# Kernel tuning notes

Hardware: AMD Instinct MI355X
Metric: run time of the kernel (lower is better)

The kernel has to match this reference:

```python
import jax, jax.numpy as jnp
import numpy as np

NEG = -1e9  # stands in for float('-inf'); exp(NEG)==0 exactly in fp32, keeps grads NaN-free
EPS = 1e-5  # torch_struct matrix-tree regularizer


def _lstm_bwd_dir(x, lengths, W_ih, W_hh, b_ih, b_hh):
    """Backward direction of a PyTorch bidirectional LSTM over packed sequences.
    x: [N,S,D], lengths: [N]. Returns y: [N,S,H] where y[n,t] is the reverse-direction
    hidden state at position t (zeros for t >= lengths[n], matching pad_packed_sequence)."""
    N, S, D = x.shape
    Hh = W_hh.shape[1]
    k = jnp.arange(S)
    idx = jnp.clip(lengths[:, None] - 1 - k[None, :], 0, S - 1)  # reverse-within-length gather
    valid = k[None, :] < lengths[:, None]                        # [N,S]
    xr = jnp.take_along_axis(x, idx[:, :, None], axis=1) * valid[..., None]

    def step(carry, inp):
        h, c = carry
        xt, vt = inp
        gates = xt @ W_ih.T + h @ W_hh.T + (b_ih + b_hh)
        i, f, g, o = jnp.split(gates, 4, axis=-1)  # PyTorch gate order i,f,g,o
        c_new = jax.nn.sigmoid(f) * c + jax.nn.sigmoid(i) * jnp.tanh(g)
        h_new = jax.nn.sigmoid(o) * jnp.tanh(c_new)
        m = vt[:, None]
        return (jnp.where(m, h_new, h), jnp.where(m, c_new, c)), jnp.where(m, h_new, 0.0)

    init = (jnp.zeros((N, Hh), x.dtype), jnp.zeros((N, Hh), x.dtype))
    _, hr = jax.lax.scan(step, init, (jnp.swapaxes(xr, 0, 1), valid.T))
    hr = jnp.swapaxes(hr, 0, 1)  # [N,S,H], in reversed coordinates
    return jnp.take_along_axis(hr, idx[:, :, None], axis=1) * valid[..., None]


def _contextualize(pv, lengths, pf, pb):
    B, S, _, H = pv.shape
    rows = pv.reshape(B * S, S, H)
    # rows_f: flipped rows, lengths [S, S-1, ..., 1] per batch, rnn_b reverse-dir
    len_rf = jnp.tile(S - jnp.arange(S), B)
    rows_f = jnp.flip(_lstm_bwd_dir(jnp.flip(rows, 1), len_rf, *pb), 1)
    # rows_b: dialogue lengths, rnn_f reverse-dir
    len_rb = jnp.repeat(lengths, S)
    rows_b = _lstm_bwd_dir(rows, len_rb, *pf)
    rows_out = jnp.concatenate([rows_f, rows_b], -1).reshape(B, S, S, 2 * H)
    cols = jnp.swapaxes(pv, 1, 2).reshape(B * S, S, H)
    # cols_b: lengths [1, 2, ..., S] per batch, rnn_b reverse-dir
    len_cb = jnp.tile(jnp.arange(1, S + 1), B)
    cols_b = _lstm_bwd_dir(cols, len_cb, *pb)
    # cols_f: flipped cols, full length S, rnn_f reverse-dir
    len_cf = jnp.full((B * S,), S, dtype=jnp.int32)
    cols_f = jnp.flip(_lstm_bwd_dir(jnp.flip(cols, 1), len_cf, *pf), 1)
    cols_out = jnp.concatenate([cols_f, cols_b], -1).reshape(B, S, S, 2 * H)
    return rows_out + jnp.swapaxes(cols_out, 1, 2)


def _apply_mask(pt, lengths):
    B, T, S, _ = pt.shape
    eye = jnp.eye(S, dtype=bool)
    t_idx = jnp.arange(T)[:, None, None]
    pt = jnp.where((t_idx < T - 1) & eye, NEG, pt)                      # no non-root types on diag
    pt = jnp.where((t_idx == T - 1) & jnp.triu(jnp.ones((S, S), bool), 1), NEG, pt)  # root type only on diag
    col_pad = jnp.arange(S)[None, :] >= lengths[:, None]                 # [B,S]
    pt = jnp.where(col_pad[:, None, None, :], NEG, pt)                   # length mask on columns
    pt = jnp.where(~jnp.triu(jnp.ones((S, S), bool)), NEG, pt)           # only i <= j arcs
    return pt


def _deptree_partition(scores, lengths):
    # matrix-tree theorem partition (torch_struct NonProjectiveDependencyCRF, multiroot)
    B, S, _ = scores.shape
    valid = jnp.arange(S)[None, :] < lengths[:, None]
    scores = jnp.where(valid[:, :, None] & valid[:, None, :], scores, NEG)
    A = jnp.exp(scores) + EPS
    A = jnp.where(jnp.eye(S, dtype=bool), 0.0, A)
    lap = -A + jnp.eye(S, dtype=scores.dtype) * A.sum(axis=1)[:, None, :]  # diag(colsum) - A
    lap = lap.at[:, 0, :].set(jnp.exp(jnp.diagonal(scores, axis1=-2, axis2=-1)))  # root row
    lap = lap + jnp.eye(S, dtype=scores.dtype) * (~valid).astype(scores.dtype)[:, None, :]  # padded dims -> det*1
    return jnp.linalg.slogdet(lap)[1]


def _expand_matrix(pt):
    B, T, S, _ = pt.shape
    m = pt.reshape(B * T, S, S)
    d = jnp.diagonal(m, axis1=-2, axis2=-1)                # [BT,S]
    me = jnp.concatenate([d[:, None, :], m], axis=1)       # [BT,S+1,S]
    pad = jnp.full((B * T, S + 1, 1), NEG, pt.dtype)
    me = jnp.concatenate([pad, me], axis=2)                # [BT,S+1,S+1]
    me = jnp.where(jnp.eye(S + 1, dtype=bool), 0.0, me)
    return me.reshape(B, T, S + 1, S + 1)


def _forward(B, S, lengths, struct_vec, Wih_f, Whh_f, bih_f, bhh_f, Wih_b, Whh_b, bih_b, bhh_b, Wt, bt):
    H = struct_vec.shape[-1]
    ti, tj = np.triu_indices(S)
    pv = jnp.zeros((B, S, S, H), struct_vec.dtype).at[:, ti, tj].set(struct_vec)
    pv = _contextualize(pv, lengths, (Wih_f, Whh_f, bih_f, bhh_f), (Wih_b, Whh_b, bih_b, bhh_b))
    pt = jnp.einsum('bijd,td->btij', pv, Wt) + bt[None, :, None, None]  # Linear + permute(0,3,1,2)
    pt = _apply_mask(pt, lengths)
    labeled = jax.nn.logsumexp(pt, axis=1)                 # [B,S,S]
    logZ = _deptree_partition(labeled, lengths)
    pe = _expand_matrix(pt)
    return pe, logZ


def setup_inputs() -> dict:
    B, S, H, T = 8, 64, 512, 17
    key = jax.random.key(0)
    ks = jax.random.split(key, 12)
    s = 1.0 / np.sqrt(H)
    s2 = 1.0 / np.sqrt(2 * H)
    u = lambda k, shape, sc: jax.random.uniform(k, shape, jnp.float32, -sc, sc)
    return {
        'batch_size': B,
        'seq_len': S,
        'context_sentence_masks': jax.random.randint(ks[0], (B,), S // 2, S + 1),
        'struct_vec': jax.random.normal(ks[1], (B, S * (S + 1) // 2, H), jnp.float32),
        'input_labels': 1,
        'Wih_f': u(ks[2], (4 * H, H), s), 'Whh_f': u(ks[3], (4 * H, H), s),
        'bih_f': u(ks[4], (4 * H,), s), 'bhh_f': u(ks[5], (4 * H,), s),
        'Wih_b': u(ks[6], (4 * H, H), s), 'Whh_b': u(ks[7], (4 * H, H), s),
        'bih_b': u(ks[8], (4 * H,), s), 'bhh_b': u(ks[9], (4 * H,), s),
        'Wt': u(ks[10], (T, 2 * H), s2), 'bt': u(ks[11], (T,), s2),
    }


def reference(batch_size, seq_len, context_sentence_masks, struct_vec, input_labels,
              Wih_f, Whh_f, bih_f, bhh_f, Wih_b, Whh_b, bih_b, bhh_b, Wt, bt):
    return _forward(batch_size, seq_len, context_sentence_masks, struct_vec,
                    Wih_f, Whh_f, bih_f, bhh_f, Wih_b, Whh_b, bih_b, bhh_b, Wt, bt)
```

## Files before the change

kernel.cpp:

```cpp
#include <hip/hip_runtime.h>
#include <hip/hip_bf16.h>
#include <math.h>

#define NEGF (-1000000000.0f)

constexpr int Bc = 8;
constexpr int Sc = 64;
constexpr int Hc = 512;
constexpr int Tc = 17;
constexpr int TRIc = Sc*(Sc+1)/2;
constexpr int PTN  = Bc*Tc*Sc*Sc;

typedef __bf16 bf16x8 __attribute__((ext_vector_type(8)));
typedef float  f32x4  __attribute__((ext_vector_type(4)));

__device__ __forceinline__ int tri_idx(int i, int j){
  return i*Sc - (i*(i-1))/2 + (j - i);
}

__device__ __forceinline__ void posmap(int pass, int r, int k, int L,
                                       int& i, int& j, bool& act){
  if      (pass == 0){ act = (r < L - k);            i = r;     j = L - 1 - k; }
  else if (pass == 1){ act = (r < L - k);            i = r;     j = r + k;     }
  else if (pass == 2){ act = (r >= k) && (r < L);    i = r - k; j = r;         }
  else               { act = (r >= k) && (r < L);    i = k;     j = r;         }
  if (!act){ i = 0; j = 0; }
}

__device__ __forceinline__ float pt_val(const float* __restrict__ pt_acc,
                                        const float* __restrict__ btv,
                                        int b, int t, int i, int j, int L){
  const bool masked = (i > j) || (j >= L) ||
                      (t < Tc-1 && i == j) || (t == Tc-1 && i < j);
  if (masked) return NEGF;
  const size_t idx = (((size_t)b*Tc + t)*Sc + i)*Sc + j;
  return pt_acc[idx] + pt_acc[PTN + idx] + pt_acc[2*PTN + idx]
       + pt_acc[3*PTN + idx] + btv[t];
}

__global__ __launch_bounds__(256) void k_cvt(const float* __restrict__ s,
                                             __hip_bfloat16* __restrict__ d, int n4){
  int i = blockIdx.x*256 + threadIdx.x;
  if (i >= n4) return;
  float4 v = reinterpret_cast<const float4*>(s)[i];
  union { __hip_bfloat16 h[4]; ushort4 u; } p;
  p.h[0] = __float2bfloat16(v.x); p.h[1] = __float2bfloat16(v.y);
  p.h[2] = __float2bfloat16(v.z); p.h[3] = __float2bfloat16(v.w);
  reinterpret_cast<ushort4*>(d)[i] = p.u;
}

__global__ __launch_bounds__(256) void k_pack(
    const float* __restrict__ Whh_f, const float* __restrict__ Wih_f,
    const float* __restrict__ Whh_b, const float* __restrict__ Wih_b,
    __hip_bfloat16* __restrict__ Wp)
{
  int idx = blockIdx.x*256 + threadIdx.x;
  int k4  = idx & 255;
  int row = (idx >> 8) & 63;
  int us  = (idx >> 14) & 31;
  int ws  = idx >> 19;
  int g = row >> 4, uu = row & 15;
  int srow = g*512 + us*16 + uu;
  int k = k4*4;
  const float* src;
  if (ws == 0) src = (k < 512) ? Whh_f : Wih_f;
  else         src = (k < 512) ? Whh_b : Wih_b;
  float4 v = *reinterpret_cast<const float4*>(src + (size_t)srow*512 + (k & 511));
  union { __hip_bfloat16 h[4]; ushort4 u; } p;
  p.h[0] = __float2bfloat16(v.x); p.h[1] = __float2bfloat16(v.y);
  p.h[2] = __float2bfloat16(v.z); p.h[3] = __float2bfloat16(v.w);
  *reinterpret_cast<ushort4*>(Wp + (size_t)idx*4) = p.u;
}

__global__ __launch_bounds__(512) void k_persist(
    const __hip_bfloat16* __restrict__ Wp,
    const float* __restrict__ bih_f, const float* __restrict__ bhh_f,
    const float* __restrict__ bih_b, const float* __restrict__ bhh_b,
    const __hip_bfloat16* __restrict__ svb, const float* __restrict__ Wt,
    const int* __restrict__ lens,
    __hip_bfloat16* __restrict__ H,
    float* __restrict__ pt_acc, int* __restrict__ flags)
{
  const int bid = blockIdx.x;
  const int grp = bid & 7;
  const int us  = bid >> 3;
  const int pp  = grp >> 2;
  const int bq  = grp & 3;
  const int L0 = lens[bq*2], L1 = lens[bq*2+1];
  const int kmax = (L0 > L1) ? L0 : L1;

  const float* b1 = pp ? bih_b : bih_f;
  const float* b2 = pp ? bhh_b : bhh_f;

  const int t = threadIdx.x, lane = t & 63, wv = t >> 6;
  const int c15 = lane & 15, qq = lane >> 4;
  const int ph = wv >> 2;
  const int mq = wv & 3;
  const int pass = pp ? (ph ? 2 : 1) : (ph ? 3 : 0);
  const int b_loc = mq >> 1;
  const int b  = bq*2 + b_loc;
  const int L  = b_loc ? L1 : L0;
  const int rb0 = (mq & 1)*32;

  __shared__ ushort Wlds[65536];

  {
    const __hip_bfloat16* Wpb = Wp + (((size_t)pp*32 + us)*64)*1024;
    const int row = t >> 3, c8 = t & 7;
    const int swz = (row & 7) << 4;
    #pragma unroll
    for (int q=0; q<16; ++q){
      int4 v = *reinterpret_cast<const int4*>(Wpb + (size_t)row*1024 + c8*128 + q*8);
      *reinterpret_cast<int4*>((char*)Wlds + ((row*2048 + c8*256 + q*16) ^ swz)) = v;
    }
  }

  const int u = us*16 + c15;
  const float bsI = b1[u]        + b2[u];
  const float bsF = b1[512 + u]  + b2[512 + u];
  const float bsG = b1[1024 + u] + b2[1024 + u];
  const float bsO = b1[1536 + u] + b2[1536 + u];
  const int lswz = (c15 & 7) << 4;

  int* slots = flags + grp*32;

  const int pidx = us*4 + mq;
  const int bp   = bq*2 + (pidx >> 6);
  const int rp   = pidx & 63;
  const int Lp   = (pidx >> 6) ? L1 : L0;
  const int off_wtp = (pass==0 || pass==2) ? 512 : 0;

  float creg[2][4];
  #pragma unroll
  for (int mt=0; mt<2; ++mt)
    #pragma unroll
    for (int e=0; e<4; ++e) creg[mt][e] = 0.f;

  __syncthreads();

  for (int k=0; k<kmax; ++k){
    const int cur = k & 1;

    bool act_t[2];
    #pragma unroll
    for (int mt=0; mt<2; ++mt){
      const int rbase = rb0 + mt*16;
      act_t[mt] = (pass < 2) ? (rbase < L - k)
                             : (rbase + 15 >= k && rbase < L);
    }

    if (act_t[0] || act_t[1]){
      const __hip_bfloat16* hp[2];
      const __hip_bfloat16* xp[2];
      #pragma unroll
      for (int mt=0; mt<2; ++mt){
        const int r = rb0 + mt*16 + c15;
        int i, j; bool a_;
        posmap(pass, r, k, L, i, j, a_);
        hp[mt] = H + (((size_t)cur*4 + pass)*512 + b*64 + r)*512;
        xp[mt] = svb + ((size_t)b*TRIc + tri_idx(i, j))*512;
      }

      f32x4 acc[2][4];
      #pragma unroll
      for (int mt=0; mt<2; ++mt)
        #pragma unroll
        for (int g=0; g<4; ++g) acc[mt][g] = f32x4{0.f,0.f,0.f,0.f};

      #pragma unroll 4
      for (int c=0; c<16; ++c){
        bf16x8 a[2][2];
        const int o = (c & 7)*64 + qq*8;
        #pragma unroll
        for (int mt=0; mt<2; ++mt){
          const __hip_bfloat16* p = (c < 8) ? hp[mt] : xp[mt];
          a[0][mt] = *reinterpret_cast<const bf16x8*>(p + o);
          a[1][mt] = *reinterpret_cast<const bf16x8*>(p + o + 32);
        }
        #pragma unroll
        for (int kk=0; kk<2; ++kk){
          #pragma unroll
          for (int g=0; g<4; ++g){
            const int addr = (((g*16 + c15)*2048) + (c*2 + kk)*64 + qq*16) ^ lswz;
            bf16x8 bf = *reinterpret_cast<const bf16x8*>((const char*)Wlds + addr);
            acc[0][g] = __builtin_amdgcn_mfma_f32_16x16x32_bf16(a[kk][0], bf, acc[0][g], 0,0,0);
            acc[1][g] = __builtin_amdgcn_mfma_f32_16x16x32_bf16(a[kk][1], bf, acc[1][g], 0,0,0);
          }
        }
      }

      #pragma unroll
      for (int mt=0; mt<2; ++mt){
        #pragma unroll
        for (int e=0; e<4; ++e){
          const int r = rb0 + mt*16 + qq*4 + e;
          int i, j; bool act;
          posmap(pass, r, k, L, i, j, act);
          if (act){
            float gi = acc[mt][0][e] + bsI;
            float gf = acc[mt][1][e] + bsF;
            float gg = acc[mt][2][e] + bsG;
            float go = acc[mt][3][e] + bsO;
            float ii = 1.f/(1.f + expf(-gi));
            float ff = 1.f/(1.f + expf(-gf));
            float gt = tanhf(gg);
            float oo = 1.f/(1.f + expf(-go));
            float cn = ff*creg[mt][e] + ii*gt;
            creg[mt][e] = cn;
            float hv = oo*tanhf(cn);
            H[(((size_t)(cur^1)*4 + pass)*512 + b*64 + r)*512 + u] = __float2bfloat16(hv);
          }
        }
      }
    }

    __syncthreads();
    if (wv == 0){
      if (lane == 0)
        __hip_atomic_store(&slots[us], k + 1, __ATOMIC_RELAXED,
                           __HIP_MEMORY_SCOPE_AGENT);
      for (;;){
        int v = 0x7fffffff;
        if (lane < 32)
          v = __hip_atomic_load(&slots[lane], __ATOMIC_RELAXED,
                                __HIP_MEMORY_SCOPE_AGENT);
        if (__all(v >= k + 1)) break;
        __builtin_amdgcn_s_sleep(2);
      }
      asm volatile("buffer_inv sc0\n\ts_waitcnt vmcnt(0)" ::: "memory");
    }
    __syncthreads();

    if (k < Lp){
      int pi, pj; bool pact;
      posmap(pass, rp, k, Lp, pi, pj, pact);
      if (pact){
        const __hip_bfloat16* hrow =
            H + (((size_t)(cur^1)*4 + pass)*512 + bp*64 + rp)*512;
        bf16x8 hv8 = *reinterpret_cast<const bf16x8*>(hrow + lane*8);
        float hf[8];
        #pragma unroll
        for (int e=0; e<8; ++e) hf[e] = (float)hv8[e];
        float part[Tc];
        #pragma unroll
        for (int tt=0; tt<Tc; ++tt){
          const float* w = Wt + (size_t)tt*1024 + off_wtp + lane*8;
          float4 w0 = *reinterpret_cast<const float4*>(w);
          float4 w1 = *reinterpret_cast<const float4*>(w + 4);
          part[tt] = hf[0]*w0.x + hf[1]*w0.y + hf[2]*w0.z + hf[3]*w0.w
                   + hf[4]*w1.x + hf[5]*w1.y + hf[6]*w1.z + hf[7]*w1.w;
        }
        float* ptp = pt_acc + (size_t)(us & 3)*PTN;
        #pragma unroll
        for (int tt=0; tt<Tc; ++tt){
          float s = part[tt];
          s += __shfl_xor(s, 1);  s += __shfl_xor(s, 2);  s += __shfl_xor(s, 4);
          s += __shfl_xor(s, 8);  s += __shfl_xor(s, 16); s += __shfl_xor(s, 32);
          if (lane == tt)
            atomicAdd(&ptp[(((size_t)bp*Tc + tt)*Sc + pi)*Sc + pj], s);
        }
      }
    }
  }
}

__global__ void k_lse(const float* __restrict__ pt_acc, const float* __restrict__ btv,
                      const int* __restrict__ lens, float* __restrict__ lab){
  const int idx = blockIdx.x*256 + threadIdx.x;
  const int b = idx >> 12, ij = idx & 4095;
  const int i = ij >> 6, j = ij & 63;
  const int L = lens[b];
  float vs[Tc]; float m = -INFINITY;
  #pragma unroll
  for (int t=0;t<Tc;t++){ vs[t] = pt_val(pt_acc, btv, b, t, i, j, L); m = fmaxf(m, vs[t]); }
  float ssum = 0.f;
  #pragma unroll
  for (int t=0;t<Tc;t++) ssum += expf(vs[t]-m);
  lab[idx] = m + logf(ssum);
}

__global__ __launch_bounds__(256) void k_logz(
    const float* __restrict__ lab, const int* __restrict__ lens,
    float* __restrict__ out)
{
  __shared__ double Md[64][65];
  __shared__ double part[4][64];
  __shared__ double rootv[64];
  const int b = blockIdx.x;
  const int L = lens[b];
  const int tid = threadIdx.x;
  const int c  = tid & 63;
  const int rg = tid >> 6;

  for (int r = rg; r < 64; r += 4){
    float lv = lab[((size_t)b*Sc + r)*Sc + c];
    double a;
    if (r == c) a = 0.0;
    else { a = 1e-5; if (r < L && c < L) a += exp((double)lv); }
    Md[r][c] = a;
  }
  if (rg == 0) rootv[c] = (c < L) ? exp((double)lab[((size_t)b*Sc + c)*Sc + c]) : 0.0;
  __syncthreads();
  {
    double ps = 0.0;
    for (int r = rg; r < 64; r += 4) ps += Md[r][c];
    part[rg][c] = ps;
  }
  __syncthreads();
  const double cs = part[0][c] + part[1][c] + part[2][c] + part[3][c];
  for (int r = rg; r < 64; r += 4){
    double v;
    if (r == 0) v = rootv[c];
    else { v = -Md[r][c]; if (r == c) v += cs + ((c >= L) ? 1.0 : 0.0); }
    Md[r][c] = v;
  }
  __syncthreads();

  double logdet = 0.0;
  for (int p = 0; p < 64; ++p){
    const double diag = Md[p][p];
    logdet += log(fabs(diag));
    if (c > p){
      const double inv = 1.0/diag;
      const double mpc = Md[p][c];
      for (int r = p + 1 + rg; r < 64; r += 4)
        Md[r][c] -= Md[r][p]*inv*mpc;
    }
    __syncthreads();
  }
  if (tid == 0) out[(size_t)Bc*Tc*65*65 + b] = (float)logdet;
}

__global__ void k_out(const float* __restrict__ pt_acc, const float* __restrict__ btv,
                      const int* __restrict__ lens, float* __restrict__ out){
  const int idx = blockIdx.x*256 + threadIdx.x;
  if (idx >= Bc*Tc*65*65) return;
  const int cc = idx % 65; int tmp = idx / 65;
  const int rr = tmp % 65; tmp /= 65;
  const int t  = tmp % Tc; const int b = tmp / Tc;
  float v;
  if (rr == cc) v = 0.f;
  else if (cc == 0) v = NEGF;
  else {
    const int i = (rr == 0) ? (cc-1) : (rr-1);
    v = pt_val(pt_acc, btv, b, t, i, cc-1, lens[b]);
  }
  out[idx] = v;
}

__global__ void k_zero_out(float* out, int n){
  int i = blockIdx.x*256 + threadIdx.x;
  if (i < n) out[i] = 0.f;
}

extern "C" void kernel_launch(void* const* d_in, const int* in_sizes, int n_in,
                              void* d_out, int out_size, void* d_ws, size_t ws_size,
                              hipStream_t stream)
{
  (void)in_sizes; (void)n_in;
  const int*   lens  = (const int*)  d_in[2];
  const float* sv    = (const float*)d_in[3];
  const float* Wih_f = (const float*)d_in[5];
  const float* Whh_f = (const float*)d_in[6];
  const float* bih_f = (const float*)d_in[7];
  const float* bhh_f = (const float*)d_in[8];
  const float* Wih_b = (const float*)d_in[9];
  const float* Whh_b = (const float*)d_in[10];
  const float* bih_b = (const float*)d_in[11];
  const float* bhh_b = (const float*)d_in[12];
  const float* Wt    = (const float*)d_in[13];
  const float* btv   = (const float*)d_in[14];

  const size_t SVB  = (size_t)Bc*TRIc*Hc*2;
  const size_t WPB  = (size_t)2*32*64*1024*2;
  const size_t PT4  = (size_t)4*PTN*4;
  const size_t HB   = (size_t)2*4*512*512*2;
  const size_t LAB  = (size_t)Bc*Sc*Sc*4;
  const size_t CNT  = 1024;
  const size_t NEED = SVB + WPB + PT4 + HB + LAB + CNT + 8192;

  if (ws_size < NEED) {
    k_zero_out<<<dim3((out_size+255)/256), 256, 0, stream>>>((float*)d_out, out_size);
    return;
  }

  char* base = (char*)d_ws;
  size_t off = 0;
  auto take = [&](size_t bytes)->char*{
    char* r = base + off; off += (bytes + 255) & ~(size_t)255; return r; };

  __hip_bfloat16* svb = (__hip_bfloat16*)take(SVB);
  __hip_bfloat16* Wp  = (__hip_bfloat16*)take(WPB);
  float* pt_acc = (float*)take(PT4);
  __hip_bfloat16* H = (__hip_bfloat16*)take(HB);
  float* lab = (float*)take(LAB);
  int*   flags = (int*)take(CNT);

  (void)hipMemsetAsync(pt_acc, 0, PT4 + HB + LAB + CNT, stream);

  k_cvt <<<dim3(8320), 256, 0, stream>>>(sv, svb, 2129920);
  k_pack<<<dim3(4096), 256, 0, stream>>>(Whh_f, Wih_f, Whh_b, Wih_b, Wp);

  k_persist<<<dim3(256), 512, 0, stream>>>(Wp, bih_f, bhh_f, bih_b, bhh_b,
                                           svb, Wt, lens, H, pt_acc, flags);

  k_lse <<<dim3(128), 256, 0, stream>>>(pt_acc, btv, lens, lab);
  k_logz<<<dim3(Bc), 256, 0, stream>>>(lab, lens, (float*)d_out);
  k_out <<<dim3((Bc*Tc*65*65 + 255)/256), 256, 0, stream>>>(pt_acc, btv, lens, (float*)d_out);
}
```

Before: 1.122 ms.

## Precompute input projection for all unique struct vectors before the recurrent loop

Adds a separate GEMM kernel that computes the input-to-hidden gate contributions W_ih·x once for every unique triangular struct vector, for both directions, and stores them in bf16. The persistent recurrent kernel then only multiplies by W_hh, halving its per-step MFMA work and its LDS weight footprint. Each step instead gathers the precomputed gate values per row. The change removes redundant input projections repeated across the four passes. In exchange it adds an extra launch, a large intermediate buffer, and bf16 rounding of the precomputed gates. It also preloads all H fragments into registers, which raises register pressure.

```diff
diff --git a/kernel.cpp b/kernel.cpp
--- a/kernel.cpp
+++ b/kernel.cpp
@@ -16,6 +16,11 @@
 
 __device__ __forceinline__ int tri_idx(int i, int j){
   return i*Sc - (i*(i-1))/2 + (j - i);
+}
+
+__device__ __forceinline__ float bfu(ushort s){
+  union { ushort u; __hip_bfloat16 h; } x; x.u = s;
+  return __bfloat162float(x.h);
 }
 
 __device__ __forceinline__ void posmap(int pass, int r, int k, int L,
@@ -72,11 +77,73 @@
   *reinterpret_cast<ushort4*>(Wp + (size_t)idx*4) = p.u;
 }
 
+__global__ __launch_bounds__(512) void k_gemm_G(
+    const __hip_bfloat16* __restrict__ Wp,
+    const __hip_bfloat16* __restrict__ svb,
+    __hip_bfloat16* __restrict__ G)
+{
+  const int m0 = blockIdx.x * 128;
+  const int us = blockIdx.y;
+  const int ws = blockIdx.z;
+  const int t = threadIdx.x, lane = t & 63, wv = t >> 6;
+  const int c15 = lane & 15, qq = lane >> 4;
+
+  __shared__ ushort Wlds[32768];
+
+  {
+    const __hip_bfloat16* Wpb = Wp + (((size_t)ws*32 + us)*64)*1024 + 512;
+    const int row = t >> 3, c8 = t & 7;
+    const int swz = (row & 7) << 4;
+    #pragma unroll
+    for (int q=0; q<8; ++q){
+      int4 v = *reinterpret_cast<const int4*>(Wpb + (size_t)row*1024 + c8*64 + q*8);
+      *reinterpret_cast<int4*>((char*)Wlds + ((row*1024 + c8*128 + q*16) ^ swz)) = v;
+    }
+  }
+  __syncthreads();
+  const int lswz = (c15 & 7) << 4;
+
+  const int arow = m0 + wv*16 + c15;
+  const __hip_bfloat16* xp = svb + (size_t)arow*512;
+
+  f32x4 acc[4];
+  #pragma unroll
+  for (int g=0; g<4; ++g) acc[g] = f32x4{0.f,0.f,0.f,0.f};
+
+  #pragma unroll
+  for (int c=0; c<8; ++c){
+    const int o = c*64 + qq*8;
+    bf16x8 a0 = *reinterpret_cast<const bf16x8*>(xp + o);
+    bf16x8 a1 = *reinterpret_cast<const bf16x8*>(xp + o + 32);
+    #pragma unroll
+    for (int g=0; g<4; ++g){
+      const int ad0 = (((g*16 + c15)*1024) + (c*2+0)*64 + qq*16) ^ lswz;
+      const int ad1 = (((g*16 + c15)*1024) + (c*2+1)*64 + qq*16) ^ lswz;
+      acc[g] = __builtin_amdgcn_mfma_f32_16x16x32_bf16(
+          a0, *reinterpret_cast<const bf16x8*>((const char*)Wlds + ad0), acc[g], 0,0,0);
+      acc[g] = __builtin_amdgcn_mfma_f32_16x16x32_bf16(
+          a1, *reinterpret_cast<const bf16x8*>((const char*)Wlds + ad1), acc[g], 0,0,0);
+    }
+  }
+
+  __hip_bfloat16* Gb = G + ((size_t)ws*32 + us)*16640*64;
+  #pragma unroll
+  for (int e=0; e<4; ++e){
+    const int row = m0 + wv*16 + qq*4 + e;
+    union { __hip_bfloat16 h[4]; ushort4 u; } pk;
+    pk.h[0] = __float2bfloat16(acc[0][e]);
+    pk.h[1] = __float2bfloat16(acc[1][e]);
+    pk.h[2] = __float2bfloat16(acc[2][e]);
+    pk.h[3] = __float2bfloat16(acc[3][e]);
+    *reinterpret_cast<ushort4*>(Gb + (size_t)row*64 + c15*4) = pk.u;
+  }
+}
+
 __global__ __launch_bounds__(512) void k_persist(
     const __hip_bfloat16* __restrict__ Wp,
     const float* __restrict__ bih_f, const float* __restrict__ bhh_f,
     const float* __restrict__ bih_b, const float* __restrict__ bhh_b,
-    const __hip_bfloat16* __restrict__ svb, const float* __restrict__ Wt,
+    const __hip_bfloat16* __restrict__ G, const float* __restrict__ Wt,
     const int* __restrict__ lens,
     __hip_bfloat16* __restrict__ H,
     float* __restrict__ pt_acc, int* __restrict__ flags)
@@ -102,16 +169,16 @@
   const int L  = b_loc ? L1 : L0;
   const int rb0 = (mq & 1)*32;
 
-  __shared__ ushort Wlds[65536];
+  __shared__ ushort Wlds[32768];
 
   {
     const __hip_bfloat16* Wpb = Wp + (((size_t)pp*32 + us)*64)*1024;
     const int row = t >> 3, c8 = t & 7;
     const int swz = (row & 7) << 4;
     #pragma unroll
-    for (int q=0; q<16; ++q){
-      int4 v = *reinterpret_cast<const int4*>(Wpb + (size_t)row*1024 + c8*128 + q*8);
-      *reinterpret_cast<int4*>((char*)Wlds + ((row*2048 + c8*256 + q*16) ^ swz)) = v;
+    for (int q=0; q<8; ++q){
+      int4 v = *reinterpret_cast<const int4*>(Wpb + (size_t)row*1024 + c8*64 + q*8);
+      *reinterpret_cast<int4*>((char*)Wlds + ((row*1024 + c8*128 + q*16) ^ swz)) = v;
     }
   }
 
@@ -122,6 +189,8 @@
   const float bsO = b1[1536 + u] + b2[1536 + u];
   const int lswz = (c15 & 7) << 4;
 
+  const __hip_bfloat16* Gb = G + ((size_t)pp*32 + us)*16640*64;
+
   int* slots = flags + grp*32;
 
   const int pidx = us*4 + mq;
@@ -151,14 +220,19 @@
 
     if (act_t[0] || act_t[1]){
       const __hip_bfloat16* hp[2];
-      const __hip_bfloat16* xp[2];
       #pragma unroll
-      for (int mt=0; mt<2; ++mt){
-        const int r = rb0 + mt*16 + c15;
-        int i, j; bool a_;
-        posmap(pass, r, k, L, i, j, a_);
-        hp[mt] = H + (((size_t)cur*4 + pass)*512 + b*64 + r)*512;
-        xp[mt] = svb + ((size_t)b*TRIc + tri_idx(i, j))*512;
+      for (int mt=0; mt<2; ++mt)
+        hp[mt] = H + (((size_t)cur*4 + pass)*512 + b*64 + rb0 + mt*16 + c15)*512;
+
+      bf16x8 av[8][2][2];
+      #pragma unroll
+      for (int c=0; c<8; ++c){
+        const int o = c*64 + qq*8;
+        #pragma unroll
+        for (int mt=0; mt<2; ++mt){
+          av[c][0][mt] = *reinterpret_cast<const bf16x8*>(hp[mt] + o);
+          av[c][1][mt] = *reinterpret_cast<const bf16x8*>(hp[mt] + o + 32);
+        }
       }
 
       f32x4 acc[2][4];
@@ -167,24 +241,16 @@
         #pragma unroll
         for (int g=0; g<4; ++g) acc[mt][g] = f32x4{0.f,0.f,0.f,0.f};
 
-      #pragma unroll 4
-      for (int c=0; c<16; ++c){
-        bf16x8 a[2][2];
-        const int o = (c & 7)*64 + qq*8;
-        #pragma unroll
-        for (int mt=0; mt<2; ++mt){
-          const __hip_bfloat16* p = (c < 8) ? hp[mt] : xp[mt];
-          a[0][mt] = *reinterpret_cast<const bf16x8*>(p + o);
-          a[1][mt] = *reinterpret_cast<const bf16x8*>(p + o + 32);
-        }
+      #pragma unroll
+      for (int c=0; c<8; ++c){
         #pragma unroll
         for (int kk=0; kk<2; ++kk){
           #pragma unroll
           for (int g=0; g<4; ++g){
-            const int addr = (((g*16 + c15)*2048) + (c*2 + kk)*64 + qq*16) ^ lswz;
+            const int addr = (((g*16 + c15)*1024) + (c*2 + kk)*64 + qq*16) ^ lswz;
             bf16x8 bf = *reinterpret_cast<const bf16x8*>((const char*)Wlds + addr);
-            acc[0][g] = __builtin_amdgcn_mfma_f32_16x16x32_bf16(a[kk][0], bf, acc[0][g], 0,0,0);
-            acc[1][g] = __builtin_amdgcn_mfma_f32_16x16x32_bf16(a[kk][1], bf, acc[1][g], 0,0,0);
+            acc[0][g] = __builtin_amdgcn_mfma_f32_16x16x32_bf16(av[c][kk][0], bf, acc[0][g], 0,0,0);
+            acc[1][g] = __builtin_amdgcn_mfma_f32_16x16x32_bf16(av[c][kk][1], bf, acc[1][g], 0,0,0);
           }
         }
       }
@@ -197,10 +263,12 @@
           int i, j; bool act;
           posmap(pass, r, k, L, i, j, act);
           if (act){
-            float gi = acc[mt][0][e] + bsI;
-            float gf = acc[mt][1][e] + bsF;
-            float gg = acc[mt][2][e] + bsG;
-            float go = acc[mt][3][e] + bsO;
+            const size_t grow = (size_t)b*TRIc + tri_idx(i, j);
+            const ushort4 gu = *reinterpret_cast<const ushort4*>(Gb + grow*64 + c15*4);
+            float gi = acc[mt][0][e] + bsI + bfu(gu.x);
+            float gf = acc[mt][1][e] + bsF + bfu(gu.y);
+            float gg = acc[mt][2][e] + bsG + bfu(gu.z);
+            float go = acc[mt][3][e] + bsO + bfu(gu.w);
             float ii = 1.f/(1.f + expf(-gi));
             float ff = 1.f/(1.f + expf(-gf));
             float gt = tanhf(gg);
@@ -373,11 +441,12 @@
 
   const size_t SVB  = (size_t)Bc*TRIc*Hc*2;
   const size_t WPB  = (size_t)2*32*64*1024*2;
+  const size_t GB   = (size_t)2*32*16640*64*2;
   const size_t PT4  = (size_t)4*PTN*4;
   const size_t HB   = (size_t)2*4*512*512*2;
   const size_t LAB  = (size_t)Bc*Sc*Sc*4;
-  const size_t CNT  = 1024;
-  const size_t NEED = SVB + WPB + PT4 + HB + LAB + CNT + 8192;
+  const size_t FLG  = 1024;
+  const size_t NEED = SVB + WPB + GB + PT4 + HB + LAB + FLG + 8192;
 
   if (ws_size < NEED) {
     k_zero_out<<<dim3((out_size+255)/256), 256, 0, stream>>>((float*)d_out, out_size);
@@ -391,18 +460,20 @@
 
   __hip_bfloat16* svb = (__hip_bfloat16*)take(SVB);
   __hip_bfloat16* Wp  = (__hip_bfloat16*)take(WPB);
+  __hip_bfloat16* G   = (__hip_bfloat16*)take(GB);
   float* pt_acc = (float*)take(PT4);
   __hip_bfloat16* H = (__hip_bfloat16*)take(HB);
   float* lab = (float*)take(LAB);
-  int*   flags = (int*)take(CNT);
-
-  (void)hipMemsetAsync(pt_acc, 0, PT4 + HB + LAB + CNT, stream);
-
-  k_cvt <<<dim3(8320), 256, 0, stream>>>(sv, svb, 2129920);
-  k_pack<<<dim3(4096), 256, 0, stream>>>(Whh_f, Wih_f, Whh_b, Wih_b, Wp);
+  int*   flags = (int*)take(FLG);
+
+  (void)hipMemsetAsync(pt_acc, 0, PT4 + HB + LAB + FLG, stream);
+
+  k_cvt  <<<dim3(8320), 256, 0, stream>>>(sv, svb, 2129920);
+  k_pack <<<dim3(4096), 256, 0, stream>>>(Whh_f, Wih_f, Whh_b, Wih_b, Wp);
+  k_gemm_G<<<dim3(130, 32, 2), 512, 0, stream>>>(Wp, svb, G);
 
   k_persist<<<dim3(256), 512, 0, stream>>>(Wp, bih_f, bhh_f, bih_b, bhh_b,
-                                           svb, Wt, lens, H, pt_acc, flags);
+                                           G, Wt, lens, H, pt_acc, flags);
 
   k_lse <<<dim3(128), 256, 0, stream>>>(pt_acc, btv, lens, lab);
   k_logz<<<dim3(Bc), 256, 0, stream>>>(lab, lens, (float*)d_out);
```

After: 1.416 ms. 26.2% more time.
